# Performance work log

Hardware: AMD Instinct MI355X
Metric: run time of the kernel (lower is better)

Reference implementation:

```python
import math
import jax, jax.numpy as jnp
import numpy as np


def _median_torch_style(t):
    # torch: flatten, sort, average the middle two if even length
    s = jnp.sort(t.ravel())
    L = s.shape[0]
    if L % 2 == 0:
        m = L // 2
        return (s[m - 1] + s[m]) * 0.5
    else:
        return s[(L - 1) // 2]


def setup_inputs() -> dict:
    key = jax.random.key(0)
    kx, ky = jax.random.split(key)
    N, M, d = 4096, 4096, 64
    X = jax.random.normal(kx, (N, d), dtype=jnp.float32)
    Y = jax.random.normal(ky, (M, d), dtype=jnp.float32)
    return {"X": X, "Y": Y}


def reference(X, Y):
    # (same math as diag(XX)/diag(YY) in the original, without the wasted GEMMs)
    XY = X @ Y.T                                  # [N, M]
    x_sq = jnp.sum(X * X, axis=1)                 # [N] == diag(X X^T)
    y_sq = jnp.sum(Y * Y, axis=1)                 # [M] == diag(Y Y^T)
    dnorm2 = -2.0 * XY + x_sq[:, None] + y_sq[None, :]

    # h is None in this configuration -> median bandwidth heuristic
    med = _median_torch_style(jax.lax.stop_gradient(dnorm2))
    h = med / (2.0 * jnp.float32(math.log(X.shape[0])))
    gamma = 1.0 / (2.0 * h)
    K_XY = jnp.exp(-gamma * dnorm2)
    return K_XY
```

## Files before the change

### kernel.cpp

```cpp
#include <hip/hip_runtime.h>
#include <math.h>

#define NROWS 4096
#define DDIM  64
#define NBINS 2048
#define NSHARD 8
#define HIST_W    0.25f
#define HIST_INVW 4.0f


typedef __attribute__((ext_vector_type(8))) short short8;
typedef __attribute__((ext_vector_type(4))) float f32x4;

__device__ inline unsigned short f2bf(float f) {
    unsigned u = __builtin_bit_cast(unsigned, f);
    u += 0x7FFFu + ((u >> 16) & 1u);
    return (unsigned short)(u >> 16);
}
__device__ inline float bf2f(unsigned short h) {
    unsigned u = ((unsigned)h) << 16;
    return __builtin_bit_cast(float, u);
}

__global__ void prep_kernel(const float* __restrict__ X, const float* __restrict__ Y,
                            unsigned short* __restrict__ Xh, unsigned short* __restrict__ Xl,
                            unsigned short* __restrict__ Yh, unsigned short* __restrict__ Yl,
                            float* __restrict__ x_sq, float* __restrict__ y_sq,
                            unsigned* __restrict__ hist8, unsigned* __restrict__ ticket,
                            unsigned* __restrict__ flag) {
    int gid = blockIdx.x * blockDim.x + threadIdx.x;
    if (gid < NSHARD * NBINS) hist8[gid] = 0u;
    if (gid == 0) { *ticket = 0u; *flag = 0u; }
    int row = gid >> 3, kb = gid & 7;
    int r = (row < NROWS) ? row : row - NROWS;
    const float* src = ((row < NROWS) ? X : Y) + (size_t)r * DDIM + kb * 8;
    unsigned short* dh = (row < NROWS) ? Xh : Yh;
    unsigned short* dl = (row < NROWS) ? Xl : Yl;
    float* sq = (row < NROWS) ? x_sq : y_sq;

    float4 a = *(const float4*)src;
    float4 b = *(const float4*)(src + 4);
    float v[8] = {a.x, a.y, a.z, a.w, b.x, b.y, b.z, b.w};
    short8 vh, vl;
    float s = 0.f;
#pragma unroll
    for (int j = 0; j < 8; ++j) {
        s = fmaf(v[j], v[j], s);
        unsigned short h = f2bf(v[j]);
        vh[j] = (short)h;
        vl[j] = (short)f2bf(v[j] - bf2f(h));
    }
    s += __shfl_xor(s, 1);
    s += __shfl_xor(s, 2);
    s += __shfl_xor(s, 4);
    if (kb == 0) sq[r] = s;
    size_t o = ((size_t)(r >> 4) * 8 + kb) * 128 + (size_t)(r & 15) * 8;
    *(short8*)(dh + o) = vh;
    *(short8*)(dl + o) = vl;
}

template <bool FULL, typename F>
__device__ inline void compute_tile(const unsigned short* __restrict__ Xh, const unsigned short* __restrict__ Xl,
                                    const unsigned short* __restrict__ Yh, const unsigned short* __restrict__ Yl,
                                    int i0, int j0, size_t la, F&& body) {
    const int pa0 = i0 >> 4, pb0 = j0 >> 4;
    f32x4 acc[4][4];
#pragma unroll
    for (int r = 0; r < 4; ++r)
#pragma unroll
        for (int c = 0; c < 4; ++c) acc[r][c] = (f32x4){0.f, 0.f, 0.f, 0.f};

    auto step = [&](const unsigned short* A, const unsigned short* B, int kh) {
        short8 af[4], bg[4];
#pragma unroll
        for (int g = 0; g < 4; ++g) {
            af[g] = *(const short8*)(A + ((size_t)(pa0 + g) * 8 + kh * 4) * 128 + la);
            bg[g] = *(const short8*)(B + ((size_t)(pb0 + g) * 8 + kh * 4) * 128 + la);
        }
#pragma unroll
        for (int r = 0; r < 4; ++r)
#pragma unroll
            for (int c = 0; c < 4; ++c)
                acc[r][c] = __builtin_amdgcn_mfma_f32_16x16x32_bf16(af[r], bg[c], acc[r][c], 0, 0, 0);
    };
    step(Xh, Yh, 0); step(Xh, Yh, 1);
    if (FULL) {
        step(Xl, Yh, 0); step(Xl, Yh, 1);
        step(Xh, Yl, 0); step(Xh, Yl, 1);
        step(Xl, Yl, 0); step(Xl, Yl, 1);
    }
    body(acc);
}

__launch_bounds__(256, 2)
__global__ void hist_kernel(const unsigned short* __restrict__ Xh, const unsigned short* __restrict__ Xl,
                            const unsigned short* __restrict__ Yh, const unsigned short* __restrict__ Yl,
                            const float* __restrict__ x_sq, const float* __restrict__ y_sq,
                            unsigned* __restrict__ hist8) {
    __shared__ unsigned lhist[NBINS];
    const int t    = threadIdx.x;
    const int wave = t >> 6;
    const int lane = t & 63;
    const int fr = lane & 15;
    const int rb = (lane >> 4) * 4;
    const size_t la = (size_t)lane * 8;
    const int i0 = blockIdx.y * 128 + (wave >> 1) * 64;
    const int j0 = blockIdx.x * 1024 + (blockIdx.y & 7) * 128 + (wave & 1) * 64;

#pragma unroll
    for (int i = 0; i < NBINS / 256; ++i) lhist[t + i * 256] = 0u;
    __syncthreads();

    float xsv[4][4];
#pragma unroll
    for (int r = 0; r < 4; ++r)
#pragma unroll
        for (int q = 0; q < 4; ++q) xsv[r][q] = x_sq[i0 + r * 16 + rb + q];
    float ysv[4];
#pragma unroll
    for (int c = 0; c < 4; ++c) ysv[c] = y_sq[j0 + c * 16 + fr];

    compute_tile<false>(Xh, Xl, Yh, Yl, i0, j0, la, [&](f32x4 (&acc)[4][4]) {
#pragma unroll
        for (int r = 0; r < 4; ++r)
#pragma unroll
            for (int q = 0; q < 4; ++q) {
                float xs = xsv[r][q];
#pragma unroll
                for (int c = 0; c < 4; ++c) {
                    float dv = fmaf(-2.f, acc[r][c][q], xs + ysv[c]);
                    int idx = (int)(dv * HIST_INVW);
                    idx = idx < 0 ? 0 : (idx > NBINS - 1 ? NBINS - 1 : idx);
                    atomicAdd(&lhist[idx], 1u);
                }
            }
    });
    __syncthreads();
    unsigned* dst = hist8 + (size_t)((blockIdx.y * gridDim.x + blockIdx.x) & (NSHARD - 1)) * NBINS;
#pragma unroll
    for (int i = 0; i < NBINS / 256; ++i) {
        unsigned cv = lhist[t + i * 256];
        if (cv) atomicAdd(&dst[t + i * 256], cv);
    }
}

__launch_bounds__(256, 2)
__global__ void write_kernel(const unsigned short* __restrict__ Xh, const unsigned short* __restrict__ Xl,
                             const unsigned short* __restrict__ Yh, const unsigned short* __restrict__ Yl,
                             const float* __restrict__ x_sq, const float* __restrict__ y_sq,
                             const unsigned* __restrict__ hist8, unsigned* __restrict__ ticket,
                             unsigned* __restrict__ flag, unsigned* __restrict__ params,
                             float* __restrict__ out) {
    __shared__ float T[4][64][68];
    __shared__ int s_red;
    __shared__ float s_cc;
    const int t    = threadIdx.x;
    const int wave = t >> 6;
    const int lane = t & 63;
    const int fr = lane & 15;
    const int rb = (lane >> 4) * 4;
    const size_t la = (size_t)lane * 8;
    const int i0 = blockIdx.y * 128 + (wave >> 1) * 64;
    const int j0 = blockIdx.x * 128 + (wave & 1) * 64;

    if (t == 0) s_red = (atomicAdd(ticket, 1u) == 0u);
    __syncthreads();

    if (s_red) {
        unsigned* cnt  = (unsigned*)&T[0][0][0];
        unsigned* tsum = cnt + NBINS;
        float*    vmed = (float*)(tsum + 256);
        unsigned s = 0;
#pragma unroll
        for (int i = 0; i < NBINS / 256; ++i) {
            unsigned b = t * (NBINS / 256) + i;
            unsigned cv = 0;
#pragma unroll
            for (int sd = 0; sd < NSHARD; ++sd)
                cv += hist8[sd * NBINS + b];
            cnt[b] = cv;
            s += cv;
        }
        tsum[t] = s;
        __syncthreads();
        for (int off = 1; off < 256; off <<= 1) {
            unsigned v = (t >= off) ? tsum[t - off] : 0u;
            __syncthreads();
            tsum[t] += v;
            __syncthreads();
        }
        unsigned cum = (t == 0) ? 0u : tsum[t - 1];
        unsigned total = tsum[255];
        const unsigned K2 = total >> 1;
        const unsigned K1 = K2 - 1u + (total & 1u);
        for (int i = 0; i < NBINS / 256; ++i) {
            int b = t * (NBINS / 256) + i;
            unsigned cv = cnt[b];
            if (cv) {
                if (K1 >= cum && (K1 - cum) < cv) {
                    float frac = ((float)(K1 - cum) + 0.5f) / (float)cv;
                    vmed[0] = ((float)b + frac) * HIST_W;
                }
                if (K2 >= cum && (K2 - cum) < cv) {
                    float frac = ((float)(K2 - cum) + 0.5f) / (float)cv;
                    vmed[1] = ((float)b + frac) * HIST_W;
                }
            }
            cum += cv;
        }
        __syncthreads();
        if (t == 0) {
            double med   = 0.5 * ((double)vmed[0] + (double)vmed[1]);
            double gamma = 8.317766166719343 / med;
            float  c     = (float)(-gamma * 1.4426950408889634);
            atomicExch(params, __builtin_bit_cast(unsigned, c));
            __threadfence();
            atomicExch(flag, 1u);
        }
        __syncthreads();
    }

    float xsv[4][4];
#pragma unroll
    for (int r = 0; r < 4; ++r)
#pragma unroll
        for (int q = 0; q < 4; ++q) xsv[r][q] = x_sq[i0 + r * 16 + rb + q];
    float ysv[4];
#pragma unroll
    for (int c = 0; c < 4; ++c) ysv[c] = y_sq[j0 + c * 16 + fr];

    compute_tile<true>(Xh, Xl, Yh, Yl, i0, j0, la, [&](f32x4 (&acc)[4][4]) {
        if (t == 0) {
            while (atomicAdd(flag, 0u) == 0u) __builtin_amdgcn_s_sleep(8);
            s_cc = __builtin_bit_cast(float, atomicAdd(params, 0u));
        }
        __syncthreads();
        const float cc = s_cc;

        float* Tw = &T[wave][0][0];
#pragma unroll
        for (int r = 0; r < 4; ++r)
#pragma unroll
            for (int c = 0; c < 4; ++c)
#pragma unroll
                for (int q = 0; q < 4; ++q) {
                    float dv = fmaf(-2.f, acc[r][c][q], xsv[r][q] + ysv[c]);
                    Tw[(r * 16 + rb + q) * 68 + c * 16 + fr] = __builtin_amdgcn_exp2f(cc * dv);
                }
#pragma unroll
        for (int ii = 0; ii < 16; ++ii) {
            int row = ii * 4 + (lane >> 4);
            f32x4 v = *(const f32x4*)&Tw[row * 68 + fr * 4];
            f32x4* po = (f32x4*)(out + (size_t)(i0 + row) * NROWS + j0 + fr * 4);
            __builtin_nontemporal_store(v, po);
        }
    });
}

extern "C" void kernel_launch(void* const* d_in, const int* in_sizes, int n_in,
                              void* d_out, int out_size, void* d_ws, size_t ws_size,
                              hipStream_t stream) {
    const float* X = (const float*)d_in[0];
    const float* Y = (const float*)d_in[1];
    float* out = (float*)d_out;

    unsigned* hist8    = (unsigned*)d_ws;
    float* x_sq        = (float*)((char*)d_ws + 65536);
    float* y_sq        = (float*)((char*)d_ws + 81920);
    unsigned* params   = (unsigned*)((char*)d_ws + 98304);
    unsigned* ticket   = (unsigned*)((char*)d_ws + 98308);
    unsigned* flag     = (unsigned*)((char*)d_ws + 98312);
    unsigned short* Xh = (unsigned short*)((char*)d_ws + 131072);
    unsigned short* Xl = Xh + (size_t)NROWS * DDIM;
    unsigned short* Yh = Xl + (size_t)NROWS * DDIM;
    unsigned short* Yl = Yh + (size_t)NROWS * DDIM;

    prep_kernel<<<256, 256, 0, stream>>>(X, Y, Xh, Xl, Yh, Yl, x_sq, y_sq, hist8, ticket, flag);
    hist_kernel<<<dim3(4, 32), 256, 0, stream>>>(Xh, Xl, Yh, Yl, x_sq, y_sq, hist8);
    write_kernel<<<dim3(32, 32), 256, 0, stream>>>(Xh, Xl, Yh, Yl, x_sq, y_sq,
                                                   hist8, ticket, flag, params, out);
}
```

Baseline: 41.92 us.

## Fuse prep, histogram and write kernels into one persistent 256-block kernel

Replaces the three kernels (bf16 split prep, histogram, write) with a single kernel of 256 blocks. Each block handles four output tiles and converts fp32 to hi/lo bf16 inline, also computing the row norms by shuffles. One in eight blocks builds the histogram, the last block to finish computes the median, and all blocks spin on a flag before writing exp values. A memset replaces the zeroing done in prep. This removes launch overhead and the intermediate bf16 buffers, but conversion work is repeated per tile and correctness relies on all 256 blocks being co-resident while they spin.

New measurement: 66.14 us. +57.8%, slower.

```diff
diff --git a/kernel.cpp b/kernel.cpp
--- a/kernel.cpp
+++ b/kernel.cpp
@@ -4,7 +4,8 @@
 #define NROWS 4096
 #define DDIM  64
 #define NBINS 2048
-#define NSHARD 8
+#define NSHARD 4
+#define GRID   256
 #define HIST_W    0.25f
 #define HIST_INVW 4.0f
 
@@ -22,166 +23,144 @@
     return __builtin_bit_cast(float, u);
 }
 
-__global__ void prep_kernel(const float* __restrict__ X, const float* __restrict__ Y,
-                            unsigned short* __restrict__ Xh, unsigned short* __restrict__ Xl,
-                            unsigned short* __restrict__ Yh, unsigned short* __restrict__ Yl,
-                            float* __restrict__ x_sq, float* __restrict__ y_sq,
-                            unsigned* __restrict__ hist8, unsigned* __restrict__ ticket,
-                            unsigned* __restrict__ flag) {
-    int gid = blockIdx.x * blockDim.x + threadIdx.x;
-    if (gid < NSHARD * NBINS) hist8[gid] = 0u;
-    if (gid == 0) { *ticket = 0u; *flag = 0u; }
-    int row = gid >> 3, kb = gid & 7;
-    int r = (row < NROWS) ? row : row - NROWS;
-    const float* src = ((row < NROWS) ? X : Y) + (size_t)r * DDIM + kb * 8;
-    unsigned short* dh = (row < NROWS) ? Xh : Yh;
-    unsigned short* dl = (row < NROWS) ? Xl : Yl;
-    float* sq = (row < NROWS) ? x_sq : y_sq;
-
-    float4 a = *(const float4*)src;
-    float4 b = *(const float4*)(src + 4);
-    float v[8] = {a.x, a.y, a.z, a.w, b.x, b.y, b.z, b.w};
-    short8 vh, vl;
-    float s = 0.f;
-#pragma unroll
-    for (int j = 0; j < 8; ++j) {
-        s = fmaf(v[j], v[j], s);
-        unsigned short h = f2bf(v[j]);
-        vh[j] = (short)h;
-        vl[j] = (short)f2bf(v[j] - bf2f(h));
-    }
-    s += __shfl_xor(s, 1);
-    s += __shfl_xor(s, 2);
-    s += __shfl_xor(s, 4);
-    if (kb == 0) sq[r] = s;
-    size_t o = ((size_t)(r >> 4) * 8 + kb) * 128 + (size_t)(r & 15) * 8;
-    *(short8*)(dh + o) = vh;
-    *(short8*)(dl + o) = vl;
-}
-
-template <bool FULL, typename F>
-__device__ inline void compute_tile(const unsigned short* __restrict__ Xh, const unsigned short* __restrict__ Xl,
-                                    const unsigned short* __restrict__ Yh, const unsigned short* __restrict__ Yl,
-                                    int i0, int j0, size_t la, F&& body) {
-    const int pa0 = i0 >> 4, pb0 = j0 >> 4;
-    f32x4 acc[4][4];
+template <bool FULL>
+__device__ inline void tile_pass(const float* __restrict__ X, const float* __restrict__ Y,
+                                 int i0, int j0, int lane,
+                                 f32x4 (&acc)[4][4], float (&xsv)[4][4], float (&ysv)[4]) {
+    const int fr = lane & 15;
+    const int kq = (lane >> 4) * 8;
+    const int rb = (lane >> 4) * 4;
+    float rsx[4] = {0.f, 0.f, 0.f, 0.f};
+    float rsy[4] = {0.f, 0.f, 0.f, 0.f};
 #pragma unroll
     for (int r = 0; r < 4; ++r)
 #pragma unroll
         for (int c = 0; c < 4; ++c) acc[r][c] = (f32x4){0.f, 0.f, 0.f, 0.f};
 
-    auto step = [&](const unsigned short* A, const unsigned short* B, int kh) {
-        short8 af[4], bg[4];
+#pragma unroll
+    for (int kh = 0; kh < 2; ++kh) {
+        short8 ah[4], al[4], bh[4], bl[4];
 #pragma unroll
         for (int g = 0; g < 4; ++g) {
-            af[g] = *(const short8*)(A + ((size_t)(pa0 + g) * 8 + kh * 4) * 128 + la);
-            bg[g] = *(const short8*)(B + ((size_t)(pb0 + g) * 8 + kh * 4) * 128 + la);
+            const float* px = X + (size_t)(i0 + g * 16 + fr) * DDIM + kh * 32 + kq;
+            const float* py = Y + (size_t)(j0 + g * 16 + fr) * DDIM + kh * 32 + kq;
+            float4 xa = *(const float4*)px, xb = *(const float4*)(px + 4);
+            float4 ya = *(const float4*)py, yb = *(const float4*)(py + 4);
+            float vx[8] = {xa.x, xa.y, xa.z, xa.w, xb.x, xb.y, xb.z, xb.w};
+            float vy[8] = {ya.x, ya.y, ya.z, ya.w, yb.x, yb.y, yb.z, yb.w};
+            short8 hx, lx, hy, ly;
+#pragma unroll
+            for (int j = 0; j < 8; ++j) {
+                rsx[g] = fmaf(vx[j], vx[j], rsx[g]);
+                rsy[g] = fmaf(vy[j], vy[j], rsy[g]);
+                unsigned short h1 = f2bf(vx[j]); hx[j] = (short)h1;
+                unsigned short h2 = f2bf(vy[j]); hy[j] = (short)h2;
+                if (FULL) {
+                    lx[j] = (short)f2bf(vx[j] - bf2f(h1));
+                    ly[j] = (short)f2bf(vy[j] - bf2f(h2));
+                }
+            }
+            ah[g] = hx; bh[g] = hy;
+            if (FULL) { al[g] = lx; bl[g] = ly; }
         }
 #pragma unroll
         for (int r = 0; r < 4; ++r)
 #pragma unroll
-            for (int c = 0; c < 4; ++c)
-                acc[r][c] = __builtin_amdgcn_mfma_f32_16x16x32_bf16(af[r], bg[c], acc[r][c], 0, 0, 0);
-    };
-    step(Xh, Yh, 0); step(Xh, Yh, 1);
-    if (FULL) {
-        step(Xl, Yh, 0); step(Xl, Yh, 1);
-        step(Xh, Yl, 0); step(Xh, Yl, 1);
-        step(Xl, Yl, 0); step(Xl, Yl, 1);
-    }
-    body(acc);
+            for (int c = 0; c < 4; ++c) {
+                acc[r][c] = __builtin_amdgcn_mfma_f32_16x16x32_bf16(ah[r], bh[c], acc[r][c], 0, 0, 0);
+                if (FULL) {
+                    acc[r][c] = __builtin_amdgcn_mfma_f32_16x16x32_bf16(al[r], bh[c], acc[r][c], 0, 0, 0);
+                    acc[r][c] = __builtin_amdgcn_mfma_f32_16x16x32_bf16(ah[r], bl[c], acc[r][c], 0, 0, 0);
+                    acc[r][c] = __builtin_amdgcn_mfma_f32_16x16x32_bf16(al[r], bl[c], acc[r][c], 0, 0, 0);
+                }
+            }
+    }
+#pragma unroll
+    for (int g = 0; g < 4; ++g) {
+        float rx = rsx[g];
+        rx += __shfl_xor(rx, 16); rx += __shfl_xor(rx, 32);
+        float ry = rsy[g];
+        ry += __shfl_xor(ry, 16); ry += __shfl_xor(ry, 32);
+#pragma unroll
+        for (int q = 0; q < 4; ++q) xsv[g][q] = __shfl(rx, rb + q);
+        ysv[g] = ry;
+    }
 }
 
 __launch_bounds__(256, 2)
-__global__ void hist_kernel(const unsigned short* __restrict__ Xh, const unsigned short* __restrict__ Xl,
-                            const unsigned short* __restrict__ Yh, const unsigned short* __restrict__ Yl,
-                            const float* __restrict__ x_sq, const float* __restrict__ y_sq,
-                            unsigned* __restrict__ hist8) {
+__global__ void fused_kernel(const float* __restrict__ X, const float* __restrict__ Y,
+                             unsigned* __restrict__ shards, unsigned* __restrict__ done,
+                             unsigned* __restrict__ flag, unsigned* __restrict__ params,
+                             float* __restrict__ out) {
+    __shared__ float T[4][64][68];
     __shared__ unsigned lhist[NBINS];
+    __shared__ unsigned tsum[256];
+    __shared__ float vmed[2];
+    __shared__ float s_cc;
+    __shared__ int s_last;
+
     const int t    = threadIdx.x;
     const int wave = t >> 6;
     const int lane = t & 63;
     const int fr = lane & 15;
     const int rb = (lane >> 4) * 4;
-    const size_t la = (size_t)lane * 8;
-    const int i0 = blockIdx.y * 128 + (wave >> 1) * 64;
-    const int j0 = blockIdx.x * 1024 + (blockIdx.y & 7) * 128 + (wave & 1) * 64;
-
-#pragma unroll
-    for (int i = 0; i < NBINS / 256; ++i) lhist[t + i * 256] = 0u;
+    const int b  = blockIdx.x;
+    const int bx = b & 31;
+    const int by0 = b >> 5;
+    const bool duty = (((by0 + bx) & 7) == 0);
+
+    if (duty) {
+#pragma unroll
+        for (int i = 0; i < NBINS / 256; ++i) lhist[t + i * 256] = 0u;
+        __syncthreads();
+#pragma unroll 1
+        for (int s = 0; s < 4; ++s) {
+            const int i0 = (by0 + 8 * s) * 128 + (wave >> 1) * 64;
+            const int j0 = bx * 128 + (wave & 1) * 64;
+            f32x4 acc[4][4];
+            float xsv[4][4], ysv[4];
+            tile_pass<false>(X, Y, i0, j0, lane, acc, xsv, ysv);
+#pragma unroll
+            for (int r = 0; r < 4; ++r)
+#pragma unroll
+                for (int q = 0; q < 4; ++q) {
+                    float xs = xsv[r][q];
+#pragma unroll
+                    for (int c = 0; c < 4; ++c) {
+                        float dv = fmaf(-2.f, acc[r][c][q], xs + ysv[c]);
+                        int idx = (int)(dv * HIST_INVW);
+                        idx = idx < 0 ? 0 : (idx > NBINS - 1 ? NBINS - 1 : idx);
+                        atomicAdd(&lhist[idx], 1u);
+                    }
+                }
+        }
+        __syncthreads();
+        unsigned* dst = shards + (size_t)(b & (NSHARD - 1)) * NBINS;
+#pragma unroll
+        for (int i = 0; i < NBINS / 256; ++i) {
+            unsigned cv = lhist[t + i * 256];
+            if (cv) atomicAdd(&dst[t + i * 256], cv);
+        }
+    }
+
+    __threadfence();
     __syncthreads();
-
-    float xsv[4][4];
-#pragma unroll
-    for (int r = 0; r < 4; ++r)
-#pragma unroll
-        for (int q = 0; q < 4; ++q) xsv[r][q] = x_sq[i0 + r * 16 + rb + q];
-    float ysv[4];
-#pragma unroll
-    for (int c = 0; c < 4; ++c) ysv[c] = y_sq[j0 + c * 16 + fr];
-
-    compute_tile<false>(Xh, Xl, Yh, Yl, i0, j0, la, [&](f32x4 (&acc)[4][4]) {
-#pragma unroll
-        for (int r = 0; r < 4; ++r)
-#pragma unroll
-            for (int q = 0; q < 4; ++q) {
-                float xs = xsv[r][q];
-#pragma unroll
-                for (int c = 0; c < 4; ++c) {
-                    float dv = fmaf(-2.f, acc[r][c][q], xs + ysv[c]);
-                    int idx = (int)(dv * HIST_INVW);
-                    idx = idx < 0 ? 0 : (idx > NBINS - 1 ? NBINS - 1 : idx);
-                    atomicAdd(&lhist[idx], 1u);
-                }
-            }
-    });
+    if (t == 0) s_last = (atomicAdd(done, 1u) == GRID - 1u);
     __syncthreads();
-    unsigned* dst = hist8 + (size_t)((blockIdx.y * gridDim.x + blockIdx.x) & (NSHARD - 1)) * NBINS;
-#pragma unroll
-    for (int i = 0; i < NBINS / 256; ++i) {
-        unsigned cv = lhist[t + i * 256];
-        if (cv) atomicAdd(&dst[t + i * 256], cv);
-    }
-}
-
-__launch_bounds__(256, 2)
-__global__ void write_kernel(const unsigned short* __restrict__ Xh, const unsigned short* __restrict__ Xl,
-                             const unsigned short* __restrict__ Yh, const unsigned short* __restrict__ Yl,
-                             const float* __restrict__ x_sq, const float* __restrict__ y_sq,
-                             const unsigned* __restrict__ hist8, unsigned* __restrict__ ticket,
-                             unsigned* __restrict__ flag, unsigned* __restrict__ params,
-                             float* __restrict__ out) {
-    __shared__ float T[4][64][68];
-    __shared__ int s_red;
-    __shared__ float s_cc;
-    const int t    = threadIdx.x;
-    const int wave = t >> 6;
-    const int lane = t & 63;
-    const int fr = lane & 15;
-    const int rb = (lane >> 4) * 4;
-    const size_t la = (size_t)lane * 8;
-    const int i0 = blockIdx.y * 128 + (wave >> 1) * 64;
-    const int j0 = blockIdx.x * 128 + (wave & 1) * 64;
-
-    if (t == 0) s_red = (atomicAdd(ticket, 1u) == 0u);
-    __syncthreads();
-
-    if (s_red) {
-        unsigned* cnt  = (unsigned*)&T[0][0][0];
-        unsigned* tsum = cnt + NBINS;
-        float*    vmed = (float*)(tsum + 256);
-        unsigned s = 0;
+    if (s_last) {
+        __threadfence();
+        unsigned ssum = 0;
 #pragma unroll
         for (int i = 0; i < NBINS / 256; ++i) {
-            unsigned b = t * (NBINS / 256) + i;
+            unsigned bn = t * (NBINS / 256) + i;
             unsigned cv = 0;
 #pragma unroll
             for (int sd = 0; sd < NSHARD; ++sd)
-                cv += hist8[sd * NBINS + b];
-            cnt[b] = cv;
-            s += cv;
-        }
-        tsum[t] = s;
+                cv += atomicAdd(&shards[sd * NBINS + bn], 0u);
+            lhist[bn] = cv;
+            ssum += cv;
+        }
+        tsum[t] = ssum;
         __syncthreads();
         for (int off = 1; off < 256; off <<= 1) {
             unsigned v = (t >= off) ? tsum[t - off] : 0u;
@@ -190,21 +169,17 @@
             __syncthreads();
         }
         unsigned cum = (t == 0) ? 0u : tsum[t - 1];
-        unsigned total = tsum[255];
+        const unsigned total = tsum[255];
         const unsigned K2 = total >> 1;
         const unsigned K1 = K2 - 1u + (total & 1u);
         for (int i = 0; i < NBINS / 256; ++i) {
-            int b = t * (NBINS / 256) + i;
-            unsigned cv = cnt[b];
+            int bn = t * (NBINS / 256) + i;
+            unsigned cv = lhist[bn];
             if (cv) {
-                if (K1 >= cum && (K1 - cum) < cv) {
-                    float frac = ((float)(K1 - cum) + 0.5f) / (float)cv;
-                    vmed[0] = ((float)b + frac) * HIST_W;
-                }
-                if (K2 >= cum && (K2 - cum) < cv) {
-                    float frac = ((float)(K2 - cum) + 0.5f) / (float)cv;
-                    vmed[1] = ((float)b + frac) * HIST_W;
-                }
+                if (K1 >= cum && (K1 - cum) < cv)
+                    vmed[0] = ((float)bn + ((float)(K1 - cum) + 0.5f) / (float)cv) * HIST_W;
+                if (K2 >= cum && (K2 - cum) < cv)
+                    vmed[1] = ((float)bn + ((float)(K2 - cum) + 0.5f) / (float)cv) * HIST_W;
             }
             cum += cv;
         }
@@ -220,21 +195,22 @@
         __syncthreads();
     }
 
-    float xsv[4][4];
-#pragma unroll
-    for (int r = 0; r < 4; ++r)
-#pragma unroll
-        for (int q = 0; q < 4; ++q) xsv[r][q] = x_sq[i0 + r * 16 + rb + q];
-    float ysv[4];
-#pragma unroll
-    for (int c = 0; c < 4; ++c) ysv[c] = y_sq[j0 + c * 16 + fr];
-
-    compute_tile<true>(Xh, Xl, Yh, Yl, i0, j0, la, [&](f32x4 (&acc)[4][4]) {
-        if (t == 0) {
-            while (atomicAdd(flag, 0u) == 0u) __builtin_amdgcn_s_sleep(8);
-            s_cc = __builtin_bit_cast(float, atomicAdd(params, 0u));
-        }
-        __syncthreads();
+#pragma unroll 1
+    for (int s = 0; s < 4; ++s) {
+        const int i0 = (by0 + 8 * s) * 128 + (wave >> 1) * 64;
+        const int j0 = bx * 128 + (wave & 1) * 64;
+        f32x4 acc[4][4];
+        float xsv[4][4], ysv[4];
+        tile_pass<true>(X, Y, i0, j0, lane, acc, xsv, ysv);
+
+        if (s == 0) {
+            if (t == 0) {
+                while (atomicAdd(flag, 0u) == 0u) __builtin_amdgcn_s_sleep(8);
+                __threadfence();
+                s_cc = __builtin_bit_cast(float, atomicAdd(params, 0u));
+            }
+            __syncthreads();
+        }
         const float cc = s_cc;
 
         float* Tw = &T[wave][0][0];
@@ -254,7 +230,7 @@
             f32x4* po = (f32x4*)(out + (size_t)(i0 + row) * NROWS + j0 + fr * 4);
             __builtin_nontemporal_store(v, po);
         }
-    });
+    }
 }
 
 extern "C" void kernel_launch(void* const* d_in, const int* in_sizes, int n_in,
@@ -264,19 +240,11 @@
     const float* Y = (const float*)d_in[1];
     float* out = (float*)d_out;
 
-    unsigned* hist8    = (unsigned*)d_ws;
-    float* x_sq        = (float*)((char*)d_ws + 65536);
-    float* y_sq        = (float*)((char*)d_ws + 81920);
-    unsigned* params   = (unsigned*)((char*)d_ws + 98304);
-    unsigned* ticket   = (unsigned*)((char*)d_ws + 98308);
-    unsigned* flag     = (unsigned*)((char*)d_ws + 98312);
-    unsigned short* Xh = (unsigned short*)((char*)d_ws + 131072);
-    unsigned short* Xl = Xh + (size_t)NROWS * DDIM;
-    unsigned short* Yh = Xl + (size_t)NROWS * DDIM;
-    unsigned short* Yl = Yh + (size_t)NROWS * DDIM;
-
-    prep_kernel<<<256, 256, 0, stream>>>(X, Y, Xh, Xl, Yh, Yl, x_sq, y_sq, hist8, ticket, flag);
-    hist_kernel<<<dim3(4, 32), 256, 0, stream>>>(Xh, Xl, Yh, Yl, x_sq, y_sq, hist8);
-    write_kernel<<<dim3(32, 32), 256, 0, stream>>>(Xh, Xl, Yh, Yl, x_sq, y_sq,
-                                                   hist8, ticket, flag, params, out);
-}
+    unsigned* shards = (unsigned*)d_ws;
+    unsigned* done   = (unsigned*)((char*)d_ws + 32768);
+    unsigned* flag   = (unsigned*)((char*)d_ws + 32772);
+    unsigned* params = (unsigned*)((char*)d_ws + 32776);
+
+    hipMemsetAsync(d_ws, 0, 32780, stream);
+    fused_kernel<<<GRID, 256, 0, stream>>>(X, Y, shards, done, flag, params, out);
+}
```
